# Performance work log

Measured on AMD Instinct MI355X. Metric: run time of the kernel, lower is better.

## Reference

```python
import jax, jax.numpy as jnp
import numpy as np

B, T, G, P = 16, 256, 1024, 16          # batch, num_tf, num_genes, peaks per gene
N, GO_DIM = 4096, 6                      # num_gos, go_dim (hard-coded in module)
HEADS, OUT_CH = 2, 4                     # selfGATConv(go_dim, 4, heads=2)
E = 65536                                # num edges
NUM_OUT = 32


def lrelu(x, slope):
    return jnp.where(x >= 0, x, slope * x)


def setup_inputs() -> dict:
    ks = jax.random.split(jax.random.key(0), 12)
    x = jax.random.normal(ks[0], (B, T, G * P), dtype=jnp.float32)
    edge_index = jax.random.randint(ks[1], (2, E), 0, N, dtype=jnp.int64)
    # per-gene subNet: Linear(num_peak*num_tf, 1) -> weight [G, T, P], bias [G]
    W_sub = jax.random.normal(ks[2], (G, T, P), dtype=jnp.float32) * 0.02
    b_sub = jax.random.normal(ks[3], (G,), dtype=jnp.float32) * 0.02
    fc1_weight = jax.random.normal(ks[4], (N * GO_DIM, G), dtype=jnp.float32) * 0.02
    mask = (jax.random.uniform(ks[5], (N, G)) < 0.05).astype(jnp.float32)
    mask_rep = jnp.repeat(mask, GO_DIM, axis=0)  # [N*GO_DIM, G]
    fc1_bias = jax.random.normal(ks[6], (N * GO_DIM,), dtype=jnp.float32) * 0.02
    gat_weight = jax.random.normal(ks[7], (GO_DIM, HEADS * OUT_CH), dtype=jnp.float32) * 0.3
    gat_att = jax.random.normal(ks[8], (1, 1, HEADS, 2 * OUT_CH), dtype=jnp.float32) * 0.3
    gat_bias = jax.random.normal(ks[9], (OUT_CH,), dtype=jnp.float32) * 0.02
    out_weight = jax.random.normal(ks[10], (NUM_OUT, N * OUT_CH), dtype=jnp.float32) * 0.02
    out_bias = jax.random.normal(ks[11], (NUM_OUT,), dtype=jnp.float32) * 0.02
    return {"x": x, "edge_index": edge_index, "W_sub": W_sub, "b_sub": b_sub,
            "fc1_weight": fc1_weight, "mask_rep": mask_rep, "fc1_bias": fc1_bias,
            "gat_weight": gat_weight, "gat_att": gat_att, "gat_bias": gat_bias,
            "out_weight": out_weight, "out_bias": out_bias}


def reference(x, edge_index, W_sub, b_sub, fc1_weight, mask_rep, fc1_bias,
              gat_weight, gat_att, gat_bias, out_weight, out_bias):
    # --- per-gene subnets (uniform num_peaks -> block-diag as one einsum) ---
    xg = x.reshape(B, T, G, P)                        # contiguous cut blocks
    x_cat = jnp.einsum('btgp,gtp->bg', xg, W_sub) + b_sub   # [B, G]
    x_cat = lrelu(x_cat, 0.01)                        # nn.LeakyReLU default
    # --- masked dense linear -> GO-term hidden layer ---
    h = x_cat @ (fc1_weight * mask_rep).T + fc1_bias  # [B, N*GO_DIM]
    h = lrelu(h, 0.01)
    h = h.reshape(B, GO_DIM, N).transpose(2, 0, 1)    # [N, B, GO_DIM]
    # --- selfGATConv: gather -> leaky_relu score -> seg-softmax -> scatter-mean ---
    hn = (h @ gat_weight).reshape(N, B, HEADS, OUT_CH)  # [N, B, H, C]
    src, dst = edge_index[0], edge_index[1]
    x_j = hn[src]                                     # [E, B, H, C]
    x_i = hn[dst]
    att = gat_att[0, 0]                               # [H, 2C]
    alpha = (jnp.einsum('ebhc,hc->ebh', x_i, att[:, :OUT_CH]) +
             jnp.einsum('ebhc,hc->ebh', x_j, att[:, OUT_CH:]))
    alpha = lrelu(alpha, 0.2)                         # negative_slope=0.2
    amax = jax.ops.segment_max(alpha, dst, num_segments=N)
    alpha = jnp.exp(alpha - amax[dst])
    denom = jax.ops.segment_sum(alpha, dst, num_segments=N)
    alpha = alpha / denom[dst]                        # per-destination softmax
    msg = x_j * alpha[..., None]                      # [E, B, H, C]
    summed = jax.ops.segment_sum(msg, dst, num_segments=N)
    cnt = jax.ops.segment_sum(jnp.ones((E,), jnp.float32), dst, num_segments=N)
    aggr = summed / jnp.maximum(cnt, 1.0)[:, None, None, None]  # aggr='mean'
    aggr = aggr.mean(axis=2) + gat_bias               # concat=False: mean heads -> [N, B, C]
    # --- readout ---
    o = aggr.transpose(1, 2, 0).reshape(B, OUT_CH * N)
    o = lrelu(o, 0.01)                                # dropout is identity in eval
    return o @ out_weight.T + out_bias                # [B, NUM_OUT]
```

## Files before the change

### kernel.cpp

```cpp
#include <hip/hip_runtime.h>
#include <math.h>

#define KB 16
#define KT 256
#define KG 1024
#define KP 16
#define KN 4096
#define KGO 6
#define KH 2
#define KC 4
#define KE 65536
#define KOUT 32

__device__ __forceinline__ float lrelu(float x, float s) { return x >= 0.f ? x : s * x; }

__global__ __launch_bounds__(256) void k0_detect(const int* __restrict__ e32,
                                                 int* __restrict__ flag) {
    __shared__ int nz;
    if (threadIdx.x == 0) nz = 0;
    __syncthreads();
    int any = 0;
#pragma unroll
    for (int k = 0; k < 4; ++k) {
        int idx = (threadIdx.x * 4 + k) * 2 + 1;
        any |= (e32[idx] != 0) ? 1 : 0;
    }
    if (any) atomicOr(&nz, 1);
    __syncthreads();
    if (threadIdx.x == 0) flag[0] = (nz == 0) ? 1 : 0;
}

__global__ __launch_bounds__(1024) void k1_subnet(const float* __restrict__ x,
                                                  const float* __restrict__ Wsub,
                                                  const float* __restrict__ bsub,
                                                  float* __restrict__ xcat) {
    int tid = threadIdx.x;
    int sub = tid >> 8;
    int u   = tid & 255;
    int gc  = blockIdx.x >> 4;
    int b   = blockIdx.x & 15;
    int g0  = gc * 64;
    int g   = g0 + (u >> 2);
    int p4  = (u & 3) * 4;
    const float* xb = x + (size_t)b * (KT * KG * KP) + (size_t)g0 * KP + u * 4;
    const float* wg = Wsub + (size_t)g * (KT * KP) + p4;
    float4 acc = make_float4(0.f, 0.f, 0.f, 0.f);
    int t0 = sub * 64;
#pragma unroll 4
    for (int i = 0; i < 64; ++i) {
        int t = t0 + i;
        float4 xv = *(const float4*)(xb + (size_t)t * (KG * KP));
        float4 wv = *(const float4*)(wg + (size_t)t * KP);
        acc.x += xv.x * wv.x; acc.y += xv.y * wv.y;
        acc.z += xv.z * wv.z; acc.w += xv.w * wv.w;
    }
    float s = acc.x + acc.y + acc.z + acc.w;
    s += __shfl_xor(s, 1, 64);
    s += __shfl_xor(s, 2, 64);
    __shared__ float part[4][64];
    if ((u & 3) == 0) part[sub][u >> 2] = s;
    __syncthreads();
    if (tid < 64) {
        float v = part[0][tid] + part[1][tid] + part[2][tid] + part[3][tid];
        xcat[b * KG + g0 + tid] = lrelu(v + bsub[g0 + tid], 0.01f);
    }
}

__global__ __launch_bounds__(256) void k2_fc1(const float* __restrict__ w,
                                              const float* __restrict__ mask,
                                              const float* __restrict__ bias,
                                              const float* __restrict__ xcat,
                                              float* __restrict__ ht) {
    int wid = threadIdx.x >> 6;
    int lane = threadIdx.x & 63;
    int b0 = wid * 4;
    float4 xcr[4][4];
#pragma unroll
    for (int bb = 0; bb < 4; ++bb)
#pragma unroll
        for (int i = 0; i < 4; ++i)
            xcr[bb][i] = *(const float4*)(xcat + (b0 + bb) * KG + i * 256 + lane * 4);

    for (int r = 0; r < 16; ++r) {
        int j = blockIdx.x * 16 + r;
        const float* wr = w + (size_t)j * KG;
        const float* mr = mask + (size_t)j * KG;
        float acc0 = 0.f, acc1 = 0.f, acc2 = 0.f, acc3 = 0.f;
#pragma unroll
        for (int i = 0; i < 4; ++i) {
            float4 wv = *(const float4*)(wr + i * 256 + lane * 4);
            float4 mv = *(const float4*)(mr + i * 256 + lane * 4);
            float px = wv.x * mv.x, py = wv.y * mv.y, pz = wv.z * mv.z, pw = wv.w * mv.w;
            acc0 += px * xcr[0][i].x + py * xcr[0][i].y + pz * xcr[0][i].z + pw * xcr[0][i].w;
            acc1 += px * xcr[1][i].x + py * xcr[1][i].y + pz * xcr[1][i].z + pw * xcr[1][i].w;
            acc2 += px * xcr[2][i].x + py * xcr[2][i].y + pz * xcr[2][i].z + pw * xcr[2][i].w;
            acc3 += px * xcr[3][i].x + py * xcr[3][i].y + pz * xcr[3][i].z + pw * xcr[3][i].w;
        }
#pragma unroll
        for (int m = 1; m < 64; m <<= 1) {
            acc0 += __shfl_xor(acc0, m, 64);
            acc1 += __shfl_xor(acc1, m, 64);
            acc2 += __shfl_xor(acc2, m, 64);
            acc3 += __shfl_xor(acc3, m, 64);
        }
        if (lane == 0) {
            float bj = bias[j];
            int d = j >> 12;
            int n = j & 4095;
            float* hp = ht + ((size_t)n * KB) * KGO + d;
            hp[(b0 + 0) * KGO] = lrelu(acc0 + bj, 0.01f);
            hp[(b0 + 1) * KGO] = lrelu(acc1 + bj, 0.01f);
            hp[(b0 + 2) * KGO] = lrelu(acc2 + bj, 0.01f);
            hp[(b0 + 3) * KGO] = lrelu(acc3 + bj, 0.01f);
        }
    }
}

__global__ __launch_bounds__(256) void k3_gatw(const float* __restrict__ ht,
                                               const float* __restrict__ gw,
                                               const float* __restrict__ att,
                                               float* __restrict__ hn,
                                               float* __restrict__ si,
                                               float* __restrict__ sj) {
    __shared__ float cgw[48];
    __shared__ float catt[16];
    int t = threadIdx.x;
    if (t < 48) cgw[t] = gw[t];
    else if (t < 64) catt[t - 48] = att[t - 48];
    __syncthreads();
    int idx = blockIdx.x * 256 + t;
    float h6[6];
#pragma unroll
    for (int d = 0; d < 6; ++d) h6[d] = ht[(size_t)idx * KGO + d];
    float o[8];
#pragma unroll
    for (int hc = 0; hc < 8; ++hc) {
        float v = 0.f;
#pragma unroll
        for (int d = 0; d < 6; ++d) v += h6[d] * cgw[d * 8 + hc];
        o[hc] = v;
        hn[(size_t)idx * 8 + hc] = v;
    }
#pragma unroll
    for (int hh = 0; hh < 2; ++hh) {
        float vi = 0.f, vj = 0.f;
#pragma unroll
        for (int c = 0; c < 4; ++c) {
            vi += o[hh * 4 + c] * catt[hh * 8 + c];
            vj += o[hh * 4 + c] * catt[hh * 8 + 4 + c];
        }
        si[idx * 2 + hh] = vi;
        sj[idx * 2 + hh] = vj;
    }
}

__global__ __launch_bounds__(256) void k4a_hist(const int* __restrict__ e32,
                                                const int* __restrict__ flag,
                                                int* __restrict__ cnt) {
    int e = blockIdx.x * 256 + threadIdx.x;
    int mode = flag[0];
    int d = mode ? e32[2 * (KE + e)] : e32[KE + e];
    atomicAdd(&cnt[d], 1);
}

__global__ __launch_bounds__(1024) void k4b_scan(const int* __restrict__ cnt,
                                                 int* __restrict__ off,
                                                 int* __restrict__ cur) {
    __shared__ int buf[2][1024];
    int t = threadIdx.x;
    int c0 = cnt[t * 4 + 0], c1 = cnt[t * 4 + 1], c2 = cnt[t * 4 + 2], c3 = cnt[t * 4 + 3];
    int s = c0 + c1 + c2 + c3;
    buf[0][t] = s;
    __syncthreads();
    int pb = 0;
    for (int d = 1; d < 1024; d <<= 1) {
        int v = buf[pb][t];
        if (t >= d) v += buf[pb][t - d];
        buf[1 - pb][t] = v;
        pb = 1 - pb;
        __syncthreads();
    }
    int incl = buf[pb][t];
    int base = incl - s;
    int o0 = base, o1 = base + c0, o2 = base + c0 + c1, o3 = base + c0 + c1 + c2;
    off[t * 4 + 0] = o0; off[t * 4 + 1] = o1; off[t * 4 + 2] = o2; off[t * 4 + 3] = o3;
    cur[t * 4 + 0] = o0; cur[t * 4 + 1] = o1; cur[t * 4 + 2] = o2; cur[t * 4 + 3] = o3;
    if (t == 1023) off[KN] = incl;
}

__global__ __launch_bounds__(256) void k4c_scatter(const int* __restrict__ e32,
                                                   const int* __restrict__ flag,
                                                   int* __restrict__ cur,
                                                   int* __restrict__ csr) {
    int e = blockIdx.x * 256 + threadIdx.x;
    int mode = flag[0];
    int d = mode ? e32[2 * (KE + e)] : e32[KE + e];
    int s = mode ? e32[2 * e] : e32[e];
    int p = atomicAdd(&cur[d], 1);
    csr[p] = s;
}

__global__ __launch_bounds__(256) void k5_gat(const int* __restrict__ offs,
                                              const int* __restrict__ csr,
                                              const float* __restrict__ si,
                                              const float* __restrict__ sj,
                                              const float* __restrict__ hn,
                                              const float* __restrict__ gbias,
                                              float* __restrict__ aggr) {
    int n = blockIdx.x;
    int t = threadIdx.x;
    int p = t >> 3;
    int s = t & 7;
    int b = p >> 1, h = p & 1;
    int off = offs[n];
    int deg = offs[n + 1] - off;
    __shared__ float red[32][4];
    float l = 0.f, a0 = 0.f, a1 = 0.f, a2 = 0.f, a3 = 0.f;
    if (deg > 0) {
        float sib = si[(n * KB + b) * 2 + h];
        float m = -1e30f;
        for (int i = s; i < deg; i += 8) {
            int sv = csr[off + i];
            float a = sib + sj[(sv * KB + b) * 2 + h];
            a = a >= 0.f ? a : 0.2f * a;
            m = fmaxf(m, a);
        }
        m = fmaxf(m, __shfl_xor(m, 1, 64));
        m = fmaxf(m, __shfl_xor(m, 2, 64));
        m = fmaxf(m, __shfl_xor(m, 4, 64));
        for (int i = s; i < deg; i += 8) {
            int sv = csr[off + i];
            float a = sib + sj[(sv * KB + b) * 2 + h];
            a = a >= 0.f ? a : 0.2f * a;
            float wgt = expf(a - m);
            l += wgt;
            float4 hv = *(const float4*)(hn + ((size_t)(sv * KB + b)) * 8 + h * 4);
            a0 += wgt * hv.x; a1 += wgt * hv.y; a2 += wgt * hv.z; a3 += wgt * hv.w;
        }
#pragma unroll
        for (int d = 1; d <= 4; d <<= 1) {
            l  += __shfl_xor(l,  d, 64);
            a0 += __shfl_xor(a0, d, 64);
            a1 += __shfl_xor(a1, d, 64);
            a2 += __shfl_xor(a2, d, 64);
            a3 += __shfl_xor(a3, d, 64);
        }
    }
    if (s == 0) {
        float inv = (deg > 0) ? 1.f / l : 0.f;
        red[p][0] = a0 * inv; red[p][1] = a1 * inv;
        red[p][2] = a2 * inv; red[p][3] = a3 * inv;
    }
    __syncthreads();
    if (t < 64) {
        int bb = t >> 2, c = t & 3;
        float v = gbias[c];
        if (deg > 0)
            v += 0.5f * (red[bb * 2 + 0][c] + red[bb * 2 + 1][c]) / (float)deg;
        aggr[bb * (KC * KN) + c * KN + n] = v;
    }
}

__global__ __launch_bounds__(256) void k6_out(const float* __restrict__ aggr,
                                              const float* __restrict__ ow,
                                              const float* __restrict__ obias,
                                              float* __restrict__ out) {
    int b = blockIdx.x >> 5;
    int k = blockIdx.x & 31;
    int t = threadIdx.x;
    const float* ar = aggr + (size_t)b * (KC * KN);
    const float* wr = ow + (size_t)k * (KC * KN);
    float sum = 0.f;
#pragma unroll 4
    for (int i = 0; i < 16; ++i) {
        int j = (i * 256 + t) * 4;
        float4 av = *(const float4*)(ar + j);
        float4 wv = *(const float4*)(wr + j);
        av.x = lrelu(av.x, 0.01f); av.y = lrelu(av.y, 0.01f);
        av.z = lrelu(av.z, 0.01f); av.w = lrelu(av.w, 0.01f);
        sum += av.x * wv.x + av.y * wv.y + av.z * wv.z + av.w * wv.w;
    }
#pragma unroll
    for (int d = 32; d > 0; d >>= 1) sum += __shfl_down(sum, d, 64);
    __shared__ float wsum[4];
    if ((t & 63) == 0) wsum[t >> 6] = sum;
    __syncthreads();
    if (t == 0) out[b * KOUT + k] = wsum[0] + wsum[1] + wsum[2] + wsum[3] + obias[k];
}

extern "C" void kernel_launch(void* const* d_in, const int* in_sizes, int n_in,
                              void* d_out, int out_size, void* d_ws, size_t ws_size,
                              hipStream_t stream) {
    const float* x     = (const float*)d_in[0];
    const int*   e32   = (const int*)d_in[1];
    const float* Wsub  = (const float*)d_in[2];
    const float* bsub  = (const float*)d_in[3];
    const float* fc1w  = (const float*)d_in[4];
    const float* maskr = (const float*)d_in[5];
    const float* fc1b  = (const float*)d_in[6];
    const float* gatw  = (const float*)d_in[7];
    const float* gata  = (const float*)d_in[8];
    const float* gatb  = (const float*)d_in[9];
    const float* outw  = (const float*)d_in[10];
    const float* outb  = (const float*)d_in[11];
    float* out = (float*)d_out;

    float* ws   = (float*)d_ws;
    float* xcat = ws;
    float* ht   = xcat + KB * KG;
    float* hn   = ht + (size_t)KN * KB * KGO;
    float* si   = hn + (size_t)KN * KB * KH * KC;
    float* sj   = si + (size_t)KN * KB * KH;
    float* aggr = sj + (size_t)KN * KB * KH;
    int* icnt  = (int*)(aggr + (size_t)KB * KC * KN);
    int* ioff  = icnt + KN;
    int* icur  = ioff + (KN + 16);
    int* icsr  = icur + KN;
    int* iflag = icsr + KE;

    k0_detect<<<1, 256, 0, stream>>>(e32, iflag);
    k1_subnet<<<256, 1024, 0, stream>>>(x, Wsub, bsub, xcat);
    k2_fc1<<<(KN * KGO) / 16, 256, 0, stream>>>(fc1w, maskr, fc1b, xcat, ht);
    k3_gatw<<<(KN * KB) / 256, 256, 0, stream>>>(ht, gatw, gata, hn, si, sj);
    hipMemsetAsync(icnt, 0, KN * sizeof(int), stream);
    k4a_hist<<<KE / 256, 256, 0, stream>>>(e32, iflag, icnt);
    k4b_scan<<<1, 1024, 0, stream>>>(icnt, ioff, icur);
    k4c_scatter<<<KE / 256, 256, 0, stream>>>(e32, iflag, icur, icsr);
    k5_gat<<<KN, 256, 0, stream>>>(ioff, icsr, si, sj, hn, gatb, aggr);
    k6_out<<<KB * KOUT, 256, 0, stream>>>(aggr, outw, outb, out);
}
```

Before: 557.1 us.

## Skip masked fc1 weight loads, shrink subnet blocks, fold int64 detection into edge kernels

The fc1 kernel loads the mask once per group of six repeated rows and skips loading weight chunks whose mask float4 is entirely zero. This cuts most fc1_weight traffic, since the mask is about 5% dense. The subnet kernel moves to 512-thread blocks covering 32 genes with deeper unrolling, doubling the grid. The separate edge-index-width detection kernel is dropped: each histogram and scatter block now infers the mode from its own slice of high words. That per-block inference can disagree between blocks and is less robust than the old global flag.

```diff
diff --git a/kernel.cpp b/kernel.cpp
--- a/kernel.cpp
+++ b/kernel.cpp
@@ -14,39 +14,23 @@
 
 __device__ __forceinline__ float lrelu(float x, float s) { return x >= 0.f ? x : s * x; }
 
-__global__ __launch_bounds__(256) void k0_detect(const int* __restrict__ e32,
-                                                 int* __restrict__ flag) {
-    __shared__ int nz;
-    if (threadIdx.x == 0) nz = 0;
-    __syncthreads();
-    int any = 0;
-#pragma unroll
-    for (int k = 0; k < 4; ++k) {
-        int idx = (threadIdx.x * 4 + k) * 2 + 1;
-        any |= (e32[idx] != 0) ? 1 : 0;
-    }
-    if (any) atomicOr(&nz, 1);
-    __syncthreads();
-    if (threadIdx.x == 0) flag[0] = (nz == 0) ? 1 : 0;
-}
-
-__global__ __launch_bounds__(1024) void k1_subnet(const float* __restrict__ x,
-                                                  const float* __restrict__ Wsub,
-                                                  const float* __restrict__ bsub,
-                                                  float* __restrict__ xcat) {
+__global__ __launch_bounds__(512) void k1_subnet(const float* __restrict__ x,
+                                                 const float* __restrict__ Wsub,
+                                                 const float* __restrict__ bsub,
+                                                 float* __restrict__ xcat) {
     int tid = threadIdx.x;
-    int sub = tid >> 8;
-    int u   = tid & 255;
+    int sub = tid >> 7;
+    int u   = tid & 127;
     int gc  = blockIdx.x >> 4;
     int b   = blockIdx.x & 15;
-    int g0  = gc * 64;
+    int g0  = gc * 32;
     int g   = g0 + (u >> 2);
     int p4  = (u & 3) * 4;
     const float* xb = x + (size_t)b * (KT * KG * KP) + (size_t)g0 * KP + u * 4;
     const float* wg = Wsub + (size_t)g * (KT * KP) + p4;
     float4 acc = make_float4(0.f, 0.f, 0.f, 0.f);
     int t0 = sub * 64;
-#pragma unroll 4
+#pragma unroll 8
     for (int i = 0; i < 64; ++i) {
         int t = t0 + i;
         float4 xv = *(const float4*)(xb + (size_t)t * (KG * KP));
@@ -57,10 +41,10 @@
     float s = acc.x + acc.y + acc.z + acc.w;
     s += __shfl_xor(s, 1, 64);
     s += __shfl_xor(s, 2, 64);
-    __shared__ float part[4][64];
+    __shared__ float part[4][32];
     if ((u & 3) == 0) part[sub][u >> 2] = s;
     __syncthreads();
-    if (tid < 64) {
+    if (tid < 32) {
         float v = part[0][tid] + part[1][tid] + part[2][tid] + part[3][tid];
         xcat[b * KG + g0 + tid] = lrelu(v + bsub[g0 + tid], 0.01f);
     }
@@ -81,20 +65,31 @@
         for (int i = 0; i < 4; ++i)
             xcr[bb][i] = *(const float4*)(xcat + (b0 + bb) * KG + i * 256 + lane * 4);
 
+    int mj_cur = -1;
+    float4 mreg[4];
     for (int r = 0; r < 16; ++r) {
         int j = blockIdx.x * 16 + r;
+        int mj = j / 6;
+        if (mj != mj_cur) {
+            const float* mr = mask + (size_t)(mj * 6) * KG;
+#pragma unroll
+            for (int i = 0; i < 4; ++i)
+                mreg[i] = *(const float4*)(mr + i * 256 + lane * 4);
+            mj_cur = mj;
+        }
         const float* wr = w + (size_t)j * KG;
-        const float* mr = mask + (size_t)j * KG;
         float acc0 = 0.f, acc1 = 0.f, acc2 = 0.f, acc3 = 0.f;
 #pragma unroll
         for (int i = 0; i < 4; ++i) {
-            float4 wv = *(const float4*)(wr + i * 256 + lane * 4);
-            float4 mv = *(const float4*)(mr + i * 256 + lane * 4);
-            float px = wv.x * mv.x, py = wv.y * mv.y, pz = wv.z * mv.z, pw = wv.w * mv.w;
-            acc0 += px * xcr[0][i].x + py * xcr[0][i].y + pz * xcr[0][i].z + pw * xcr[0][i].w;
-            acc1 += px * xcr[1][i].x + py * xcr[1][i].y + pz * xcr[1][i].z + pw * xcr[1][i].w;
-            acc2 += px * xcr[2][i].x + py * xcr[2][i].y + pz * xcr[2][i].z + pw * xcr[2][i].w;
-            acc3 += px * xcr[3][i].x + py * xcr[3][i].y + pz * xcr[3][i].z + pw * xcr[3][i].w;
+            float4 mv = mreg[i];
+            if (mv.x != 0.f || mv.y != 0.f || mv.z != 0.f || mv.w != 0.f) {
+                float4 wv = *(const float4*)(wr + i * 256 + lane * 4);
+                float px = wv.x * mv.x, py = wv.y * mv.y, pz = wv.z * mv.z, pw = wv.w * mv.w;
+                acc0 += px * xcr[0][i].x + py * xcr[0][i].y + pz * xcr[0][i].z + pw * xcr[0][i].w;
+                acc1 += px * xcr[1][i].x + py * xcr[1][i].y + pz * xcr[1][i].z + pw * xcr[1][i].w;
+                acc2 += px * xcr[2][i].x + py * xcr[2][i].y + pz * xcr[2][i].z + pw * xcr[2][i].w;
+                acc3 += px * xcr[3][i].x + py * xcr[3][i].y + pz * xcr[3][i].z + pw * xcr[3][i].w;
+            }
         }
 #pragma unroll
         for (int m = 1; m < 64; m <<= 1) {
@@ -155,10 +150,16 @@
 }
 
 __global__ __launch_bounds__(256) void k4a_hist(const int* __restrict__ e32,
-                                                const int* __restrict__ flag,
                                                 int* __restrict__ cnt) {
-    int e = blockIdx.x * 256 + threadIdx.x;
-    int mode = flag[0];
+    __shared__ int smode;
+    int t = threadIdx.x;
+    int e = blockIdx.x * 256 + t;
+    int hi = e32[2 * e + 1];
+    if (t == 0) smode = 1;
+    __syncthreads();
+    if (hi != 0) smode = 0;
+    __syncthreads();
+    int mode = smode;
     int d = mode ? e32[2 * (KE + e)] : e32[KE + e];
     atomicAdd(&cnt[d], 1);
 }
@@ -189,11 +190,17 @@
 }
 
 __global__ __launch_bounds__(256) void k4c_scatter(const int* __restrict__ e32,
-                                                   const int* __restrict__ flag,
                                                    int* __restrict__ cur,
                                                    int* __restrict__ csr) {
-    int e = blockIdx.x * 256 + threadIdx.x;
-    int mode = flag[0];
+    __shared__ int smode;
+    int t = threadIdx.x;
+    int e = blockIdx.x * 256 + t;
+    int hi = e32[2 * e + 1];
+    if (t == 0) smode = 1;
+    __syncthreads();
+    if (hi != 0) smode = 0;
+    __syncthreads();
+    int mode = smode;
     int d = mode ? e32[2 * (KE + e)] : e32[KE + e];
     int s = mode ? e32[2 * e] : e32[e];
     int p = atomicAdd(&cur[d], 1);
@@ -316,16 +323,14 @@
     int* ioff  = icnt + KN;
     int* icur  = ioff + (KN + 16);
     int* icsr  = icur + KN;
-    int* iflag = icsr + KE;
-
-    k0_detect<<<1, 256, 0, stream>>>(e32, iflag);
-    k1_subnet<<<256, 1024, 0, stream>>>(x, Wsub, bsub, xcat);
+
+    k1_subnet<<<512, 512, 0, stream>>>(x, Wsub, bsub, xcat);
     k2_fc1<<<(KN * KGO) / 16, 256, 0, stream>>>(fc1w, maskr, fc1b, xcat, ht);
     k3_gatw<<<(KN * KB) / 256, 256, 0, stream>>>(ht, gatw, gata, hn, si, sj);
     hipMemsetAsync(icnt, 0, KN * sizeof(int), stream);
-    k4a_hist<<<KE / 256, 256, 0, stream>>>(e32, iflag, icnt);
+    k4a_hist<<<KE / 256, 256, 0, stream>>>(e32, icnt);
     k4b_scan<<<1, 1024, 0, stream>>>(icnt, ioff, icur);
-    k4c_scatter<<<KE / 256, 256, 0, stream>>>(e32, iflag, icur, icsr);
+    k4c_scatter<<<KE / 256, 256, 0, stream>>>(e32, icur, icsr);
     k5_gat<<<KN, 256, 0, stream>>>(ioff, icsr, si, sj, hn, gatb, aggr);
     k6_out<<<KB * KOUT, 256, 0, stream>>>(aggr, outw, outb, out);
 }
```

Measured after the change: 602.7 us. 8.2% more time.
